# Kernel optimization log

Measured on AMD Instinct MI355X. Metric: run time of the kernel, lower is better.

Reference implementation:

```python
import jax, jax.numpy as jnp
import numpy as np

TEMPERATURE = 1.0          # args.matching_temperature default
CONSISTENCY_WEIGHT = 0.5   # args.matching_consistency_weight default
EPS = 1e-6


def setup_inputs() -> dict:
    key = jax.random.key(0)
    k1, k2, k3 = jax.random.split(key, 3)
    query = jax.random.normal(k1, (8192, 1024), dtype=jnp.float32)
    memory_bank = jax.random.normal(k2, (16384, 1024), dtype=jnp.float32)
    # per-memory-entry local density scale (mean kNN distance within the lib)
    neighbor_scale_bank = jax.random.uniform(k3, (16384,), dtype=jnp.float32) + 0.5
    return {
        "query": query,
        "memory_bank": memory_bank,
        "neighbor_scale_bank": neighbor_scale_bank,
        "k": 5,
    }


def _cdist(x, y):
    # Euclidean pairwise distances [Nq, Nm], GEMM-based like torch.cdist.
    x2 = jnp.sum(x * x, axis=1, keepdims=True)          # [Nq, 1]
    y2 = jnp.sum(y * y, axis=1)[None, :]                # [1, Nm]
    d2 = x2 + y2 - 2.0 * (x @ y.T)                      # [Nq, Nm]
    return jnp.sqrt(jnp.maximum(d2, 1e-12))


def reference(query, memory_bank, neighbor_scale_bank, k):
    # _compute_memory_matching_scores with matching_mode='adaptive_knn'
    dist = _cdist(query, memory_bank)                   # [Nq, Nm]
    k = min(k, memory_bank.shape[0])
    neg_d, knn_indices = jax.lax.top_k(-dist, k)        # k smallest distances
    knn_distances = -neg_d                              # [Nq, k]

    # _reduce_knn_distances, mode='adaptive_knn'
    weights = jax.nn.softmax(-knn_distances / TEMPERATURE, axis=1)
    weighted_distance = jnp.sum(weights * knn_distances, axis=1)  # [Nq]

    neighbor_scale = neighbor_scale_bank[knn_indices].mean(axis=1)  # [Nq]
    normalized_distance = weighted_distance / jnp.maximum(neighbor_scale, EPS)

    mean_d = knn_distances.mean(axis=1)
    consistency = knn_distances.std(axis=1) / jnp.maximum(mean_d, EPS)
    return normalized_distance * (1.0 + CONSISTENCY_WEIGHT * consistency)
```

## Files before the change

### kernel.cpp

```cpp
#include <hip/hip_runtime.h>
#include <hip/hip_bf16.h>
#include <math.h>

#define NQ   8192
#define NM   16384
#define DIM  1024
#define KNN  5

#define SPLITS 8
#define SLICE  (NM / SPLITS)
#define TILEM  128
#define TILES  (SLICE / TILEM)
#define BK     64
#define TPB1   512
#define CPQ    (SPLITS * 16 * 5)

typedef float  f32x4_t  __attribute__((ext_vector_type(4)));
typedef __bf16 bf16x8_t __attribute__((ext_vector_type(8)));

typedef __attribute__((address_space(1))) unsigned int gu32_t;
typedef __attribute__((address_space(3))) unsigned int lu32_t;

__device__ __forceinline__ void gl16(const void* g, void* l) {
    __builtin_amdgcn_global_load_lds((gu32_t*)g, (lu32_t*)l, 16, 0, 0);
}

__global__ void m2_kernel(const float* __restrict__ mem, float* __restrict__ m2) {
    const int row  = blockIdx.x * 4 + (threadIdx.x >> 6);
    const int lane = threadIdx.x & 63;
    const float4* p = reinterpret_cast<const float4*>(mem + (size_t)row * DIM) + lane;
    float s = 0.f;
#pragma unroll
    for (int i = 0; i < 4; ++i) {
        const float4 v = p[i * 64];
        s += v.x * v.x + v.y * v.y + v.z * v.z + v.w * v.w;
    }
#pragma unroll
    for (int off = 32; off > 0; off >>= 1) s += __shfl_down(s, off);
    if (lane == 0) m2[row] = s;
}

__global__ void cvt_bf16_kernel(const float* __restrict__ in,
                                __hip_bfloat16* __restrict__ out, int n8) {
    const int i = blockIdx.x * blockDim.x + threadIdx.x;
    if (i >= n8) return;
    const float4 a = reinterpret_cast<const float4*>(in)[2 * i];
    const float4 b = reinterpret_cast<const float4*>(in)[2 * i + 1];
    bf16x8_t v;
    v[0] = (__bf16)a.x; v[1] = (__bf16)a.y; v[2] = (__bf16)a.z; v[3] = (__bf16)a.w;
    v[4] = (__bf16)b.x; v[5] = (__bf16)b.y; v[6] = (__bf16)b.z; v[7] = (__bf16)b.w;
    reinterpret_cast<bf16x8_t*>(out)[i] = v;
}

__launch_bounds__(TPB1, 4)
__global__ void knn_phase1(const __hip_bfloat16* __restrict__ Qbf,
                           const __hip_bfloat16* __restrict__ Mbf,
                           const float* __restrict__ m2,
                           float* __restrict__ keyws,
                           unsigned short* __restrict__ idxws) {
    __shared__ alignas(16) __bf16 As[TILEM][BK];
    __shared__ alignas(16) __bf16 Bs[128][BK];

    const int t    = threadIdx.x;
    const int lane = t & 63;
    const int wave = t >> 6;
    const int wr   = wave >> 1;
    const int wc   = wave & 1;
    const int g4   = lane >> 4;
    const int l16  = lane & 15;

    const int bid  = blockIdx.x;
    const int qlow = bid & 7;
    const int rest = bid >> 3;
    const int sp   = rest & 7;
    const int qhi  = rest >> 3;
    const int qc   = qhi * 8 + qlow;
    const int q0   = qc * 128;
    const int mbase = sp * SLICE;

    float    tk[4][5];
    unsigned ti[4][5];
#pragma unroll
    for (int j = 0; j < 4; ++j)
#pragma unroll
        for (int r = 0; r < 5; ++r) { tk[j][r] = 3.4e38f; ti[j][r] = 0u; }

    const int srow = t >> 3;
    const int scol = (((t & 7) ^ (srow & 7)) << 3);

    const int rxa = l16 & 7;

    const f32x4_t zero = {0.f, 0.f, 0.f, 0.f};

    for (int tile = 0; tile < TILES; ++tile) {
        const int r0 = mbase + tile * TILEM;

        f32x4_t acc[2][4];
#pragma unroll
        for (int i = 0; i < 2; ++i)
#pragma unroll
            for (int j = 0; j < 4; ++j) acc[i][j] = zero;

        for (int k0 = 0; k0 < DIM; k0 += BK) {
            const __hip_bfloat16* ga = Mbf + (size_t)(r0 + srow) * DIM + k0 + scol;
            const __hip_bfloat16* gb = Qbf + (size_t)(q0 + srow) * DIM + k0 + scol;
            char* la = (char*)&As[0][0] + t * 16;
            char* lb = (char*)&Bs[0][0] + t * 16;
            gl16(ga,                la);
            gl16(ga + 64 * DIM,     la + 8192);
            gl16(gb,                lb);
            gl16(gb + 64 * DIM,     lb + 8192);
            __syncthreads();

#pragma unroll
            for (int kk = 0; kk < BK; kk += 32) {
                const int ch   = (kk >> 3) + g4;
                const int koff = ((ch ^ rxa) << 3);
                const int ar   = wr * 32 + l16;
                const int bc   = wc * 64 + l16;
                const bf16x8_t a0 = *reinterpret_cast<const bf16x8_t*>(&As[ar][koff]);
                const bf16x8_t a1 = *reinterpret_cast<const bf16x8_t*>(&As[ar + 16][koff]);
                const bf16x8_t b0 = *reinterpret_cast<const bf16x8_t*>(&Bs[bc][koff]);
                const bf16x8_t b1 = *reinterpret_cast<const bf16x8_t*>(&Bs[bc + 16][koff]);
                const bf16x8_t b2 = *reinterpret_cast<const bf16x8_t*>(&Bs[bc + 32][koff]);
                const bf16x8_t b3 = *reinterpret_cast<const bf16x8_t*>(&Bs[bc + 48][koff]);
                acc[0][0] = __builtin_amdgcn_mfma_f32_16x16x32_bf16(a0, b0, acc[0][0], 0, 0, 0);
                acc[0][1] = __builtin_amdgcn_mfma_f32_16x16x32_bf16(a0, b1, acc[0][1], 0, 0, 0);
                acc[0][2] = __builtin_amdgcn_mfma_f32_16x16x32_bf16(a0, b2, acc[0][2], 0, 0, 0);
                acc[0][3] = __builtin_amdgcn_mfma_f32_16x16x32_bf16(a0, b3, acc[0][3], 0, 0, 0);
                acc[1][0] = __builtin_amdgcn_mfma_f32_16x16x32_bf16(a1, b0, acc[1][0], 0, 0, 0);
                acc[1][1] = __builtin_amdgcn_mfma_f32_16x16x32_bf16(a1, b1, acc[1][1], 0, 0, 0);
                acc[1][2] = __builtin_amdgcn_mfma_f32_16x16x32_bf16(a1, b2, acc[1][2], 0, 0, 0);
                acc[1][3] = __builtin_amdgcn_mfma_f32_16x16x32_bf16(a1, b3, acc[1][3], 0, 0, 0);
            }
            __syncthreads();
        }

#pragma unroll
        for (int i = 0; i < 2; ++i) {
#pragma unroll
            for (int rg = 0; rg < 4; ++rg) {
                const int lr = wr * 32 + i * 16 + g4 * 4 + rg;
                const float mm = m2[r0 + lr];
                const unsigned gidx = (unsigned)(r0 + lr);
#pragma unroll
                for (int j = 0; j < 4; ++j) {
                    const float key = fmaf(-2.0f, acc[i][j][rg], mm);
                    if (key < tk[j][4]) {
                        tk[j][4] = key; ti[j][4] = gidx;
#pragma unroll
                        for (int s = 3; s >= 0; --s) {
                            const bool sw = tk[j][s] > tk[j][s + 1];
                            const float    fa = tk[j][s], fb = tk[j][s + 1];
                            const unsigned ia = ti[j][s], ib = ti[j][s + 1];
                            tk[j][s] = sw ? fb : fa; tk[j][s + 1] = sw ? fa : fb;
                            ti[j][s] = sw ? ib : ia; ti[j][s + 1] = sw ? ia : ib;
                        }
                    }
                }
            }
        }
    }

#pragma unroll
    for (int j = 0; j < 4; ++j) {
        const int col = wc * 64 + j * 16 + l16;
        const size_t base = (size_t)(q0 + col) * CPQ + sp * 80 + (wr * 4 + g4) * 5;
#pragma unroll
        for (int r = 0; r < 5; ++r) {
            keyws[base + r] = tk[j][r];
            idxws[base + r] = (unsigned short)ti[j][r];
        }
    }
}

__global__ void knn_phase2(const float* __restrict__ query,
                           const float* __restrict__ mem,
                           const float* __restrict__ nsb,
                           const float* __restrict__ keyws,
                           const unsigned short* __restrict__ idxws,
                           float* __restrict__ out) {
    const int wv   = threadIdx.x >> 6;
    const int lane = threadIdx.x & 63;
    const int row  = blockIdx.x * 4 + wv;

    __shared__ int   sel[4][16];
    __shared__ float dsel[4][16];

    float    k[10];
    unsigned id[10];
    const size_t cb = (size_t)row * CPQ;
#pragma unroll
    for (int r = 0; r < 10; ++r) {
        k[r]  = keyws[cb + r * 64 + lane];
        id[r] = (unsigned)idxws[cb + r * 64 + lane];
    }

    for (int rr = 0; rr < 16; ++rr) {
        float lm = k[0];
#pragma unroll
        for (int r = 1; r < 10; ++r) lm = fminf(lm, k[r]);
        float m = lm;
#pragma unroll
        for (int off = 32; off > 0; off >>= 1) m = fminf(m, __shfl_xor(m, off));
        const unsigned long long bal = __ballot(lm == m);
        const bool win = (lane == (int)(__ffsll((long long)bal) - 1));
        unsigned sid = 0; bool done = false;
#pragma unroll
        for (int r = 0; r < 10; ++r) {
            const bool c = win && !done && (k[r] == m);
            sid  = c ? id[r] : sid;
            k[r] = c ? 3.4e38f : k[r];
            done = done || c;
        }
        if (win) sel[wv][rr] = (int)sid;
    }
    __syncthreads();

    const int c = lane >> 2, sub = lane & 3;
    const int mi = sel[wv][c];
    const float4* qp = reinterpret_cast<const float4*>(query + (size_t)row * DIM) + sub * 64;
    const float4* mp = reinterpret_cast<const float4*>(mem + (size_t)mi * DIM) + sub * 64;
    double acc = 0.0;
#pragma unroll 4
    for (int i = 0; i < 64; ++i) {
        const float4 q4 = qp[i];
        const float4 m4 = mp[i];
        const double d0 = (double)q4.x - (double)m4.x;
        const double d1 = (double)q4.y - (double)m4.y;
        const double d2 = (double)q4.z - (double)m4.z;
        const double d3 = (double)q4.w - (double)m4.w;
        acc += d0 * d0 + d1 * d1 + d2 * d2 + d3 * d3;
    }
    acc += __shfl_xor(acc, 1);
    acc += __shfl_xor(acc, 2);
    if (sub == 0) dsel[wv][c] = (float)sqrt(fmax(acc, 1e-12));
    __syncthreads();

    if (lane == 0) {
        float dv[16]; int di[16];
#pragma unroll
        for (int i = 0; i < 16; ++i) { dv[i] = dsel[wv][i]; di[i] = sel[wv][i]; }
        float kd[KNN]; int ki[KNN];
#pragma unroll
        for (int r = 0; r < KNN; ++r) {
            float bv = 3.4e38f; int bi = 0x7fffffff; int bp = -1;
#pragma unroll
            for (int i = 0; i < 16; ++i) {
                const bool better = (dv[i] < bv) || (dv[i] == bv && di[i] < bi);
                if (better) { bv = dv[i]; bi = di[i]; bp = i; }
            }
            kd[r] = bv; ki[r] = bi;
#pragma unroll
            for (int i = 0; i < 16; ++i) if (i == bp) dv[i] = 3.4e38f;
        }
        double dmin = (double)kd[0];
#pragma unroll
        for (int r = 1; r < KNN; ++r) dmin = fmin(dmin, (double)kd[r]);
        double w[KNN], se = 0.0, wd = 0.0, sd = 0.0, sc = 0.0;
#pragma unroll
        for (int r = 0; r < KNN; ++r) {
            w[r] = exp(-((double)kd[r] - dmin));
            se += w[r];
            sd += (double)kd[r];
            sc += (double)nsb[ki[r]];
        }
#pragma unroll
        for (int r = 0; r < KNN; ++r) wd += w[r] * (double)kd[r];
        wd /= se;
        sc /= (double)KNN;
        const double nd   = wd / fmax(sc, 1e-6);
        const double mean = sd / (double)KNN;
        double var = 0.0;
#pragma unroll
        for (int r = 0; r < KNN; ++r) { const double dd = (double)kd[r] - mean; var += dd * dd; }
        var /= (double)KNN;
        const double cons = sqrt(var) / fmax(mean, 1e-6);
        out[row] = (float)(nd * (1.0 + 0.5 * cons));
    }
}

__launch_bounds__(512, 1)
__global__ void fb_knn_phase1(const float* __restrict__ query,
                              const float* __restrict__ mem,
                              const float* __restrict__ m2,
                              float* __restrict__ wkey,
                              int* __restrict__ widx) {
    __shared__ alignas(16) __bf16 Qs[128][72];
    __shared__ alignas(16) __bf16 Ms[128][72];
    __shared__ float D2[128][129];
    __shared__ float m2s[128];

    const int t    = threadIdx.x;
    const int lane = t & 63;
    const int wave = t >> 6;
    const int wr   = wave >> 1;
    const int wc   = wave & 1;

    const int mb    = blockIdx.x & 63;
    const int sp    = blockIdx.x >> 6;
    const int q0    = mb * 128;
    const int mbase = sp * 4096;

    const int srow = t & 127;
    const int sseg = t >> 7;
    const int str = t >> 2;
    const int stc = (t & 3) * 16;

    float topv[8]; int topi[8];
#pragma unroll
    for (int i = 0; i < 8; ++i) { topv[i] = 3.4e38f; topi[i] = 0; }
    float curmax = 3.4e38f;
    const f32x4_t zero = {0.f, 0.f, 0.f, 0.f};

    for (int tile = 0; tile < 32; ++tile) {
        const int c0 = mbase + tile * 128;
        if (t < 128) m2s[t] = m2[c0 + t];
        f32x4_t acc[2][4];
#pragma unroll
        for (int i = 0; i < 2; ++i)
#pragma unroll
            for (int j = 0; j < 4; ++j) acc[i][j] = zero;

        for (int k0 = 0; k0 < DIM; k0 += 64) {
            {
                const float4* qp = reinterpret_cast<const float4*>(query + (size_t)(q0 + str) * DIM + k0 + stc);
                const float4 a0 = qp[0], a1 = qp[1], a2 = qp[2], a3 = qp[3];
                const float4* mp = reinterpret_cast<const float4*>(mem + (size_t)(c0 + str) * DIM + k0 + stc);
                const float4 b0 = mp[0], b1 = mp[1], b2 = mp[2], b3 = mp[3];
                bf16x8_t qa, qb, ma, mbv;
                qa[0] = (__bf16)a0.x; qa[1] = (__bf16)a0.y; qa[2] = (__bf16)a0.z; qa[3] = (__bf16)a0.w;
                qa[4] = (__bf16)a1.x; qa[5] = (__bf16)a1.y; qa[6] = (__bf16)a1.z; qa[7] = (__bf16)a1.w;
                qb[0] = (__bf16)a2.x; qb[1] = (__bf16)a2.y; qb[2] = (__bf16)a2.z; qb[3] = (__bf16)a2.w;
                qb[4] = (__bf16)a3.x; qb[5] = (__bf16)a3.y; qb[6] = (__bf16)a3.z; qb[7] = (__bf16)a3.w;
                ma[0] = (__bf16)b0.x; ma[1] = (__bf16)b0.y; ma[2] = (__bf16)b0.z; ma[3] = (__bf16)b0.w;
                ma[4] = (__bf16)b1.x; ma[5] = (__bf16)b1.y; ma[6] = (__bf16)b1.z; ma[7] = (__bf16)b1.w;
                mbv[0] = (__bf16)b2.x; mbv[1] = (__bf16)b2.y; mbv[2] = (__bf16)b2.z; mbv[3] = (__bf16)b2.w;
                mbv[4] = (__bf16)b3.x; mbv[5] = (__bf16)b3.y; mbv[6] = (__bf16)b3.z; mbv[7] = (__bf16)b3.w;
                *reinterpret_cast<bf16x8_t*>(&Qs[str][stc])     = qa;
                *reinterpret_cast<bf16x8_t*>(&Qs[str][stc + 8]) = qb;
                *reinterpret_cast<bf16x8_t*>(&Ms[str][stc])     = ma;
                *reinterpret_cast<bf16x8_t*>(&Ms[str][stc + 8]) = mbv;
            }
            __syncthreads();
#pragma unroll
            for (int kk = 0; kk < 64; kk += 32) {
                const int koff = kk + ((lane >> 4) << 3);
                const int ar   = wr * 32 + (lane & 15);
                const bf16x8_t a0 = *reinterpret_cast<const bf16x8_t*>(&Qs[ar][koff]);
                const bf16x8_t a1 = *reinterpret_cast<const bf16x8_t*>(&Qs[ar + 16][koff]);
                const int bc = wc * 64 + (lane & 15);
                const bf16x8_t b0 = *reinterpret_cast<const bf16x8_t*>(&Ms[bc][koff]);
                const bf16x8_t b1 = *reinterpret_cast<const bf16x8_t*>(&Ms[bc + 16][koff]);
                const bf16x8_t b2 = *reinterpret_cast<const bf16x8_t*>(&Ms[bc + 32][koff]);
                const bf16x8_t b3 = *reinterpret_cast<const bf16x8_t*>(&Ms[bc + 48][koff]);
                acc[0][0] = __builtin_amdgcn_mfma_f32_16x16x32_bf16(a0, b0, acc[0][0], 0, 0, 0);
                acc[0][1] = __builtin_amdgcn_mfma_f32_16x16x32_bf16(a0, b1, acc[0][1], 0, 0, 0);
                acc[0][2] = __builtin_amdgcn_mfma_f32_16x16x32_bf16(a0, b2, acc[0][2], 0, 0, 0);
                acc[0][3] = __builtin_amdgcn_mfma_f32_16x16x32_bf16(a0, b3, acc[0][3], 0, 0, 0);
                acc[1][0] = __builtin_amdgcn_mfma_f32_16x16x32_bf16(a1, b0, acc[1][0], 0, 0, 0);
                acc[1][1] = __builtin_amdgcn_mfma_f32_16x16x32_bf16(a1, b1, acc[1][1], 0, 0, 0);
                acc[1][2] = __builtin_amdgcn_mfma_f32_16x16x32_bf16(a1, b2, acc[1][2], 0, 0, 0);
                acc[1][3] = __builtin_amdgcn_mfma_f32_16x16x32_bf16(a1, b3, acc[1][3], 0, 0, 0);
            }
            __syncthreads();
        }
#pragma unroll
        for (int i = 0; i < 2; ++i) {
            const int r0 = wr * 32 + i * 16 + ((lane >> 4) << 2);
#pragma unroll
            for (int j = 0; j < 4; ++j) {
                const int cc = wc * 64 + j * 16 + (lane & 15);
                const float mm = m2s[cc];
#pragma unroll
                for (int rg = 0; rg < 4; ++rg)
                    D2[r0 + rg][cc] = mm - 2.0f * acc[i][j][rg];
            }
        }
        __syncthreads();
        {
            const int gbase = c0 + sseg * 32;
#pragma unroll 8
            for (int cc = 0; cc < 32; ++cc) {
                const float key = D2[srow][sseg * 32 + cc];
                if (key < curmax) {
                    bool done = false;
#pragma unroll
                    for (int i = 0; i < 8; ++i) {
                        if (!done && topv[i] == curmax) {
                            topv[i] = key; topi[i] = gbase + cc; done = true;
                        }
                    }
                    curmax = topv[0];
#pragma unroll
                    for (int i = 1; i < 8; ++i) curmax = fmaxf(curmax, topv[i]);
                }
            }
        }
        __syncthreads();
    }
    const size_t base = ((size_t)(q0 + srow) * 4 + sp) * 32 + (size_t)sseg * 8;
#pragma unroll
    for (int j = 0; j < 8; ++j) { wkey[base + j] = topv[j]; widx[base + j] = topi[j]; }
}

__global__ void fb_knn_phase2(const float* __restrict__ query,
                              const float* __restrict__ mem,
                              const float* __restrict__ nsb,
                              const float* __restrict__ wkey,
                              const int* __restrict__ widx,
                              float* __restrict__ out) {
    const int wv   = threadIdx.x >> 6;
    const int lane = threadIdx.x & 63;
    const int row  = blockIdx.x * 4 + wv;
    __shared__ int   sel[4][16];
    __shared__ float dsel[4][16];

    const size_t cb = (size_t)row * 128;
    float k0 = wkey[cb + lane];
    float k1 = wkey[cb + 64 + lane];
    const int i0 = widx[cb + lane];
    const int i1 = widx[cb + 64 + lane];

    for (int r = 0; r < 16; ++r) {
        float m = fminf(k0, k1);
#pragma unroll
        for (int off = 32; off > 0; off >>= 1) m = fminf(m, __shfl_xor(m, off));
        const unsigned long long b0 = __ballot(k0 == m);
        const unsigned long long b1 = __ballot(k1 == m);
        if (b0) {
            if (lane == __ffsll(b0) - 1) { sel[wv][r] = i0; k0 = 3.4e38f; }
        } else {
            if (lane == __ffsll(b1) - 1) { sel[wv][r] = i1; k1 = 3.4e38f; }
        }
    }
    __syncthreads();

    const int c = lane >> 2, sub = lane & 3;
    const int mi = sel[wv][c];
    const float4* qp = reinterpret_cast<const float4*>(query + (size_t)row * DIM) + sub * 64;
    const float4* mp = reinterpret_cast<const float4*>(mem + (size_t)mi * DIM) + sub * 64;
    double acc = 0.0;
#pragma unroll 4
    for (int i = 0; i < 64; ++i) {
        const float4 q4 = qp[i];
        const float4 m4 = mp[i];
        const double d0 = (double)q4.x - (double)m4.x;
        const double d1 = (double)q4.y - (double)m4.y;
        const double d2 = (double)q4.z - (double)m4.z;
        const double d3 = (double)q4.w - (double)m4.w;
        acc += d0 * d0 + d1 * d1 + d2 * d2 + d3 * d3;
    }
    acc += __shfl_xor(acc, 1);
    acc += __shfl_xor(acc, 2);
    if (sub == 0) dsel[wv][c] = (float)sqrt(fmax(acc, 1e-12));
    __syncthreads();

    if (lane == 0) {
        float dv[16]; int di[16];
#pragma unroll
        for (int i = 0; i < 16; ++i) { dv[i] = dsel[wv][i]; di[i] = sel[wv][i]; }
        float kd[KNN]; int ki[KNN];
#pragma unroll
        for (int r = 0; r < KNN; ++r) {
            float bv = 3.4e38f; int bi = 0x7fffffff; int bp = -1;
#pragma unroll
            for (int i = 0; i < 16; ++i) {
                const bool better = (dv[i] < bv) || (dv[i] == bv && di[i] < bi);
                if (better) { bv = dv[i]; bi = di[i]; bp = i; }
            }
            kd[r] = bv; ki[r] = bi;
#pragma unroll
            for (int i = 0; i < 16; ++i) if (i == bp) dv[i] = 3.4e38f;
        }
        double dmin = (double)kd[0];
#pragma unroll
        for (int r = 1; r < KNN; ++r) dmin = fmin(dmin, (double)kd[r]);
        double w[KNN], se = 0.0, wd = 0.0, sd = 0.0, sc = 0.0;
#pragma unroll
        for (int r = 0; r < KNN; ++r) {
            w[r] = exp(-((double)kd[r] - dmin));
            se += w[r];
            sd += (double)kd[r];
            sc += (double)nsb[ki[r]];
        }
#pragma unroll
        for (int r = 0; r < KNN; ++r) wd += w[r] * (double)kd[r];
        wd /= se;
        sc /= (double)KNN;
        const double nd   = wd / fmax(sc, 1e-6);
        const double mean = sd / (double)KNN;
        double var = 0.0;
#pragma unroll
        for (int r = 0; r < KNN; ++r) { const double dd = (double)kd[r] - mean; var += dd * dd; }
        var /= (double)KNN;
        const double cons = sqrt(var) / fmax(mean, 1e-6);
        out[row] = (float)(nd * (1.0 + 0.5 * cons));
    }
}

extern "C" void kernel_launch(void* const* d_in, const int* in_sizes, int n_in,
                              void* d_out, int out_size, void* d_ws, size_t ws_size,
                              hipStream_t stream) {
    const float* query = (const float*)d_in[0];
    const float* mem   = (const float*)d_in[1];
    const float* nsb   = (const float*)d_in[2];
    float* out = (float*)d_out;
    char* ws = (char*)d_ws;

    const size_t offQ   = 0;
    const size_t offM   = offQ + (size_t)NQ * DIM * 2;
    const size_t offm2  = offM + (size_t)NM * DIM * 2;
    const size_t offkey = offm2 + (size_t)NM * 4;
    const size_t offidx = offkey + (size_t)NQ * CPQ * 4;
    const size_t need   = offidx + (size_t)NQ * CPQ * 2;

    if (ws_size >= need) {
        __hip_bfloat16* Qbf = (__hip_bfloat16*)(ws + offQ);
        __hip_bfloat16* Mbf = (__hip_bfloat16*)(ws + offM);
        float*          m2  = (float*)(ws + offm2);
        float*          key = (float*)(ws + offkey);
        unsigned short* idx = (unsigned short*)(ws + offidx);

        hipLaunchKernelGGL(cvt_bf16_kernel, dim3(NQ * DIM / 8 / 256), dim3(256), 0, stream,
                           query, Qbf, NQ * DIM / 8);
        hipLaunchKernelGGL(cvt_bf16_kernel, dim3(NM * DIM / 8 / 256), dim3(256), 0, stream,
                           mem, Mbf, NM * DIM / 8);
        hipLaunchKernelGGL(m2_kernel, dim3(NM / 4), dim3(256), 0, stream, mem, m2);
        hipLaunchKernelGGL(knn_phase1, dim3((NQ / 128) * SPLITS), dim3(TPB1), 0, stream,
                           Qbf, Mbf, m2, key, idx);
        hipLaunchKernelGGL(knn_phase2, dim3(NQ / 4), dim3(256), 0, stream,
                           query, mem, nsb, key, idx, out);
    } else {
        float* wkey = (float*)ws;
        int*   widx = (int*)(ws + (size_t)NQ * 128 * 4);
        float* m2   = (float*)(ws + (size_t)NQ * 128 * 8);
        hipLaunchKernelGGL(m2_kernel, dim3(NM / 4), dim3(256), 0, stream, mem, m2);
        hipLaunchKernelGGL(fb_knn_phase1, dim3((NQ / 128) * 4), dim3(512), 0, stream,
                           query, mem, m2, wkey, widx);
        hipLaunchKernelGGL(fb_knn_phase2, dim3(NQ / 4), dim3(256), 0, stream,
                           query, mem, nsb, wkey, widx, out);
    }
}
```

Baseline: 532.0 us.

## Double-buffer LDS tiles with async prefetch across flattened tile/k loop

Flattens the tile and k-step loops into one unit loop and double-buffers the A/B LDS tiles, issuing global-to-LDS loads two steps ahead with explicit vmcnt waits and raw barriers. It also caches the slice's m2 norms in shared memory and raises wave priority around the MFMA block. The aim is to hide global load latency behind MFMA work. In exchange it doubles LDS use (plus 4KB for m2s), which may reduce occupancy under the 4-blocks-per-CU launch bound.

```diff
diff --git a/kernel.cpp b/kernel.cpp
--- a/kernel.cpp
+++ b/kernel.cpp
@@ -12,6 +12,8 @@
 #define TILEM  128
 #define TILES  (SLICE / TILEM)
 #define BK     64
+#define KSTEPS (DIM / BK)
+#define UNITS  (TILES * KSTEPS)
 #define TPB1   512
 #define CPQ    (SPLITS * 16 * 5)
 
@@ -58,8 +60,9 @@
                            const float* __restrict__ m2,
                            float* __restrict__ keyws,
                            unsigned short* __restrict__ idxws) {
-    __shared__ alignas(16) __bf16 As[TILEM][BK];
-    __shared__ alignas(16) __bf16 Bs[128][BK];
+    __shared__ alignas(16) __bf16 As[2][TILEM][BK];
+    __shared__ alignas(16) __bf16 Bs[2][128][BK];
+    __shared__ float m2s[SLICE];
 
     const int t    = threadIdx.x;
     const int lane = t & 63;
@@ -78,6 +81,9 @@
     const int q0   = qc * 128;
     const int mbase = sp * SLICE;
 
+#pragma unroll
+    for (int i = 0; i < SLICE / TPB1; ++i) m2s[t + i * TPB1] = m2[mbase + t + i * TPB1];
+
     float    tk[4][5];
     unsigned ti[4][5];
 #pragma unroll
@@ -87,78 +93,99 @@
 
     const int srow = t >> 3;
     const int scol = (((t & 7) ^ (srow & 7)) << 3);
-
-    const int rxa = l16 & 7;
-
-    const f32x4_t zero = {0.f, 0.f, 0.f, 0.f};
-
-    for (int tile = 0; tile < TILES; ++tile) {
-        const int r0 = mbase + tile * TILEM;
-
-        f32x4_t acc[2][4];
-#pragma unroll
-        for (int i = 0; i < 2; ++i)
-#pragma unroll
-            for (int j = 0; j < 4; ++j) acc[i][j] = zero;
-
-        for (int k0 = 0; k0 < DIM; k0 += BK) {
-            const __hip_bfloat16* ga = Mbf + (size_t)(r0 + srow) * DIM + k0 + scol;
-            const __hip_bfloat16* gb = Qbf + (size_t)(q0 + srow) * DIM + k0 + scol;
-            char* la = (char*)&As[0][0] + t * 16;
-            char* lb = (char*)&Bs[0][0] + t * 16;
-            gl16(ga,                la);
-            gl16(ga + 64 * DIM,     la + 8192);
-            gl16(gb,                lb);
-            gl16(gb + 64 * DIM,     lb + 8192);
-            __syncthreads();
-
-#pragma unroll
-            for (int kk = 0; kk < BK; kk += 32) {
-                const int ch   = (kk >> 3) + g4;
-                const int koff = ((ch ^ rxa) << 3);
-                const int ar   = wr * 32 + l16;
-                const int bc   = wc * 64 + l16;
-                const bf16x8_t a0 = *reinterpret_cast<const bf16x8_t*>(&As[ar][koff]);
-                const bf16x8_t a1 = *reinterpret_cast<const bf16x8_t*>(&As[ar + 16][koff]);
-                const bf16x8_t b0 = *reinterpret_cast<const bf16x8_t*>(&Bs[bc][koff]);
-                const bf16x8_t b1 = *reinterpret_cast<const bf16x8_t*>(&Bs[bc + 16][koff]);
-                const bf16x8_t b2 = *reinterpret_cast<const bf16x8_t*>(&Bs[bc + 32][koff]);
-                const bf16x8_t b3 = *reinterpret_cast<const bf16x8_t*>(&Bs[bc + 48][koff]);
-                acc[0][0] = __builtin_amdgcn_mfma_f32_16x16x32_bf16(a0, b0, acc[0][0], 0, 0, 0);
-                acc[0][1] = __builtin_amdgcn_mfma_f32_16x16x32_bf16(a0, b1, acc[0][1], 0, 0, 0);
-                acc[0][2] = __builtin_amdgcn_mfma_f32_16x16x32_bf16(a0, b2, acc[0][2], 0, 0, 0);
-                acc[0][3] = __builtin_amdgcn_mfma_f32_16x16x32_bf16(a0, b3, acc[0][3], 0, 0, 0);
-                acc[1][0] = __builtin_amdgcn_mfma_f32_16x16x32_bf16(a1, b0, acc[1][0], 0, 0, 0);
-                acc[1][1] = __builtin_amdgcn_mfma_f32_16x16x32_bf16(a1, b1, acc[1][1], 0, 0, 0);
-                acc[1][2] = __builtin_amdgcn_mfma_f32_16x16x32_bf16(a1, b2, acc[1][2], 0, 0, 0);
-                acc[1][3] = __builtin_amdgcn_mfma_f32_16x16x32_bf16(a1, b3, acc[1][3], 0, 0, 0);
-            }
-            __syncthreads();
-        }
-
-#pragma unroll
-        for (int i = 0; i < 2; ++i) {
-#pragma unroll
-            for (int rg = 0; rg < 4; ++rg) {
-                const int lr = wr * 32 + i * 16 + g4 * 4 + rg;
-                const float mm = m2[r0 + lr];
-                const unsigned gidx = (unsigned)(r0 + lr);
-#pragma unroll
-                for (int j = 0; j < 4; ++j) {
-                    const float key = fmaf(-2.0f, acc[i][j][rg], mm);
-                    if (key < tk[j][4]) {
-                        tk[j][4] = key; ti[j][4] = gidx;
-#pragma unroll
-                        for (int s = 3; s >= 0; --s) {
-                            const bool sw = tk[j][s] > tk[j][s + 1];
-                            const float    fa = tk[j][s], fb = tk[j][s + 1];
-                            const unsigned ia = ti[j][s], ib = ti[j][s + 1];
-                            tk[j][s] = sw ? fb : fa; tk[j][s + 1] = sw ? fa : fb;
-                            ti[j][s] = sw ? ib : ia; ti[j][s + 1] = sw ? ia : ib;
+    const int rxa  = l16 & 7;
+
+    f32x4_t acc[2][4];
+#pragma unroll
+    for (int i = 0; i < 2; ++i)
+#pragma unroll
+        for (int j = 0; j < 4; ++j) acc[i][j] = {0.f, 0.f, 0.f, 0.f};
+
+    auto stage = [&](int s, int buf) {
+        const int tl  = s >> 4;
+        const int kk0 = (s & 15) * BK;
+        const int rr0 = mbase + tl * TILEM;
+        const __hip_bfloat16* ga = Mbf + (size_t)(rr0 + srow) * DIM + kk0 + scol;
+        const __hip_bfloat16* gb = Qbf + (size_t)(q0 + srow) * DIM + kk0 + scol;
+        char* la = (char*)&As[buf][0][0] + t * 16;
+        char* lb = (char*)&Bs[buf][0][0] + t * 16;
+        gl16(ga,            la);
+        gl16(ga + 64 * DIM, la + 8192);
+        gl16(gb,            lb);
+        gl16(gb + 64 * DIM, lb + 8192);
+    };
+
+    stage(0, 0);
+    stage(1, 1);
+
+#pragma unroll 1
+    for (int s = 0; s < UNITS; ++s) {
+        const int cur = s & 1;
+
+        if (s == UNITS - 1) asm volatile("s_waitcnt vmcnt(0)" ::: "memory");
+        else                asm volatile("s_waitcnt vmcnt(4)" ::: "memory");
+        __builtin_amdgcn_s_barrier();
+
+        __builtin_amdgcn_s_setprio(1);
+#pragma unroll
+        for (int kk = 0; kk < BK; kk += 32) {
+            const int ch   = (kk >> 3) + g4;
+            const int koff = ((ch ^ rxa) << 3);
+            const int ar   = wr * 32 + l16;
+            const int bc   = wc * 64 + l16;
+            const bf16x8_t a0 = *reinterpret_cast<const bf16x8_t*>(&As[cur][ar][koff]);
+            const bf16x8_t a1 = *reinterpret_cast<const bf16x8_t*>(&As[cur][ar + 16][koff]);
+            const bf16x8_t b0 = *reinterpret_cast<const bf16x8_t*>(&Bs[cur][bc][koff]);
+            const bf16x8_t b1 = *reinterpret_cast<const bf16x8_t*>(&Bs[cur][bc + 16][koff]);
+            const bf16x8_t b2 = *reinterpret_cast<const bf16x8_t*>(&Bs[cur][bc + 32][koff]);
+            const bf16x8_t b3 = *reinterpret_cast<const bf16x8_t*>(&Bs[cur][bc + 48][koff]);
+            acc[0][0] = __builtin_amdgcn_mfma_f32_16x16x32_bf16(a0, b0, acc[0][0], 0, 0, 0);
+            acc[0][1] = __builtin_amdgcn_mfma_f32_16x16x32_bf16(a0, b1, acc[0][1], 0, 0, 0);
+            acc[0][2] = __builtin_amdgcn_mfma_f32_16x16x32_bf16(a0, b2, acc[0][2], 0, 0, 0);
+            acc[0][3] = __builtin_amdgcn_mfma_f32_16x16x32_bf16(a0, b3, acc[0][3], 0, 0, 0);
+            acc[1][0] = __builtin_amdgcn_mfma_f32_16x16x32_bf16(a1, b0, acc[1][0], 0, 0, 0);
+            acc[1][1] = __builtin_amdgcn_mfma_f32_16x16x32_bf16(a1, b1, acc[1][1], 0, 0, 0);
+            acc[1][2] = __builtin_amdgcn_mfma_f32_16x16x32_bf16(a1, b2, acc[1][2], 0, 0, 0);
+            acc[1][3] = __builtin_amdgcn_mfma_f32_16x16x32_bf16(a1, b3, acc[1][3], 0, 0, 0);
+        }
+        __builtin_amdgcn_s_setprio(0);
+
+        asm volatile("s_waitcnt lgkmcnt(0)" ::: "memory");
+        __builtin_amdgcn_s_barrier();
+
+        if (s + 2 < UNITS) stage(s + 2, cur);
+
+        if ((s & 15) == 15) {
+            const int tl = s >> 4;
+            const int r0 = mbase + tl * TILEM;
+#pragma unroll
+            for (int i = 0; i < 2; ++i) {
+#pragma unroll
+                for (int rg = 0; rg < 4; ++rg) {
+                    const int lr = wr * 32 + i * 16 + g4 * 4 + rg;
+                    const float mm = m2s[tl * TILEM + lr];
+                    const unsigned gidx = (unsigned)(r0 + lr);
+#pragma unroll
+                    for (int j = 0; j < 4; ++j) {
+                        const float key = fmaf(-2.0f, acc[i][j][rg], mm);
+                        if (key < tk[j][4]) {
+                            tk[j][4] = key; ti[j][4] = gidx;
+#pragma unroll
+                            for (int ss = 3; ss >= 0; --ss) {
+                                const bool sw = tk[j][ss] > tk[j][ss + 1];
+                                const float    fa = tk[j][ss], fb = tk[j][ss + 1];
+                                const unsigned ia = ti[j][ss], ib = ti[j][ss + 1];
+                                tk[j][ss] = sw ? fb : fa; tk[j][ss + 1] = sw ? fa : fb;
+                                ti[j][ss] = sw ? ib : ia; ti[j][ss + 1] = sw ? ia : ib;
+                            }
                         }
                     }
                 }
             }
+#pragma unroll
+            for (int i = 0; i < 2; ++i)
+#pragma unroll
+                for (int j = 0; j < 4; ++j) acc[i][j] = {0.f, 0.f, 0.f, 0.f};
         }
     }
 
```

Measured after the change: 494.9 us. 1.07x faster.
